# Kernel tuning notes

Measured on AMD Instinct MI355X. Metric: run time of the kernel, lower is better.

## Reference

```python
import jax, jax.numpy as jnp
import numpy as np

B, T, C, HS = 8, 2048, 1024, 64


def setup_inputs() -> dict:
    key = jax.random.key(0)
    ks = jax.random.split(key, 4)
    x = jax.random.normal(ks[0], (B, T, C), dtype=jnp.float32)
    Wq = jax.random.normal(ks[1], (C, HS), dtype=jnp.float32) * (C ** -0.5)
    Wk = jax.random.normal(ks[2], (C, HS), dtype=jnp.float32) * (C ** -0.5)
    Wv = jax.random.normal(ks[3], (C, HS), dtype=jnp.float32) * (C ** -0.5)
    mask = jnp.tril(jnp.ones((T, T), dtype=jnp.int32))  # causal mask
    return {"x": x, "mask": mask, "Wq": Wq, "Wk": Wk, "Wv": Wv}


def reference(x, mask, Wq, Wk, Wv):
    # x: [B,T,C]; bias-free projections to head_size
    q = jnp.einsum("btc,ch->bth", x, Wq)
    k = jnp.einsum("btc,ch->bth", x, Wk)
    v = jnp.einsum("btc,ch->bth", x, Wv)
    # NOTE: original scales by C**-0.5 (n_embd), not head_size**-0.5
    wei = jnp.einsum("bth,bsh->bts", q, k) * (x.shape[-1] ** -0.5)
    wei = jnp.where(mask[None, :, :] == 0, -jnp.inf, wei)
    wei = jax.nn.softmax(wei, axis=-1)
    # dropout is identity in eval / p=0
    out = jnp.einsum("bts,bsh->bth", wei, v)
    return out
```

## Files before the change

kernel.cpp:

```cpp
#include <hip/hip_runtime.h>
#include <hip/hip_bf16.h>


#define B_  8
#define T_  2048
#define C_  1024
#define HS_ 64
#define MROWS (B_ * T_)

typedef __attribute__((ext_vector_type(8))) short bf16x8;
typedef __attribute__((ext_vector_type(4))) float f32x4;
typedef __attribute__((ext_vector_type(4))) float float4v;

#define SCALE_LOG2 0.04508422037445829f

__device__ __forceinline__ short f2bs(float f) {
    __hip_bfloat16 h = __float2bfloat16(f);
    short s;
    __builtin_memcpy(&s, &h, 2);
    return s;
}

__global__ void wt_kernel(const float* __restrict__ Wq,
                          const float* __restrict__ Wk,
                          const float* __restrict__ Wv,
                          __hip_bfloat16* __restrict__ Wt) {
    int m = blockIdx.x >> 6;
    int h = blockIdx.x & 63;
    const float* W = (m == 0) ? Wq : (m == 1) ? Wk : Wv;
    size_t outBase = (size_t)m * (HS_ * C_) + (size_t)h * C_;
    for (int c = threadIdx.x; c < C_; c += blockDim.x)
        Wt[outBase + c] = __float2bfloat16(W[(size_t)c * HS_ + h]);
}

__global__ __launch_bounds__(256) void proj_kernel(
    const float* __restrict__ x,
    const __hip_bfloat16* __restrict__ Wt,
    __hip_bfloat16* __restrict__ Q,
    __hip_bfloat16* __restrict__ Kp,
    __hip_bfloat16* __restrict__ Vt)
{
    const int lane = threadIdx.x & 63;
    const int wave = threadIdx.x >> 6;
    const int quad = lane >> 4;
    const int l15  = lane & 15;
    const int row0 = blockIdx.x * 64;

    f32x4 acc[4][3];
#pragma unroll
    for (int rt = 0; rt < 4; ++rt)
#pragma unroll
        for (int j = 0; j < 3; ++j)
            acc[rt][j] = (f32x4){0.f, 0.f, 0.f, 0.f};

    for (int kc = 0; kc < C_; kc += 32) {
        bf16x8 a[4];
#pragma unroll
        for (int rt = 0; rt < 4; ++rt) {
            const float4v* p = (const float4v*)
                (x + (size_t)(row0 + rt * 16 + l15) * C_ + kc + quad * 8);
            float4v f0 = p[0], f1 = p[1];
#pragma unroll
            for (int j = 0; j < 4; ++j) { a[rt][j] = f2bs(f0[j]); a[rt][4+j] = f2bs(f1[j]); }
        }
        bf16x8 b[3];
#pragma unroll
        for (int j = 0; j < 3; ++j) {
            int nt = wave * 3 + j;
            int h  = ((nt & 3) * 16) + l15;
            b[j] = *(const bf16x8*)(Wt + (size_t)(nt >> 2) * (HS_ * C_) +
                                    (size_t)h * C_ + kc + quad * 8);
        }
#pragma unroll
        for (int rt = 0; rt < 4; ++rt)
#pragma unroll
            for (int j = 0; j < 3; ++j)
                acc[rt][j] = __builtin_amdgcn_mfma_f32_16x16x32_bf16(
                    a[rt], b[j], acc[rt][j], 0, 0, 0);
    }

#pragma unroll
    for (int rt = 0; rt < 4; ++rt) {
#pragma unroll
        for (int j = 0; j < 3; ++j) {
            int nt   = wave * 3 + j;
            int mtx  = nt >> 2;
            int col  = (nt & 3) * 16 + l15;
#pragma unroll
            for (int r = 0; r < 4; ++r) {
                int row = row0 + rt * 16 + quad * 4 + r;
                __hip_bfloat16 v = __float2bfloat16(acc[rt][j][r]);
                if (mtx == 0) {
                    Q[(size_t)row * HS_ + col] = v;
                } else if (mtx == 1) {
                    Kp[(size_t)row * HS_ + col] = v;
                } else {
                    int bidx = row >> 11;
                    int t    = row & 2047;
                    Vt[((size_t)bidx * HS_ + col) * T_ + t] = v;
                }
            }
        }
    }
}

__global__ __launch_bounds__(256) void attn_kernel(
    const __hip_bfloat16* __restrict__ Q,
    const __hip_bfloat16* __restrict__ Kp,
    const __hip_bfloat16* __restrict__ Vt,
    float* __restrict__ out)
{
    __shared__ __align__(16) __hip_bfloat16 plds[4][16 * 32];
    __shared__ float o_lds[4][16][64];
    __shared__ float l_lds[4][16][16];

    const int tid  = threadIdx.x;
    const int wv   = tid >> 6;
    const int lane = tid & 63;
    const int quad = lane >> 4;
    const int l15  = lane & 15;
    const int b    = blockIdx.x & 7;
    const int lt   = 127 - (blockIdx.x >> 3);
    const int qb   = lt * 16;
    const int rowg = b * T_ + qb;

    bf16x8 qf0 = *(const bf16x8*)(Q + (size_t)(rowg + l15) * HS_ + quad * 8);
    bf16x8 qf1 = *(const bf16x8*)(Q + (size_t)(rowg + l15) * HS_ + 32 + quad * 8);

    f32x4 o[4];
#pragma unroll
    for (int j = 0; j < 4; ++j) o[j] = (f32x4){0.f, 0.f, 0.f, 0.f};
    float lp[4] = {0.f, 0.f, 0.f, 0.f};

    __hip_bfloat16* pb = plds[wv];
    const int ntiles = qb / 32 + 1;

    for (int t = wv; t < ntiles; t += 4) {
        const int kb = t * 32;
        const __hip_bfloat16* Kb = Kp + (size_t)(b * T_ + kb) * HS_;
        bf16x8 k0a = *(const bf16x8*)(Kb + (size_t)l15 * HS_ + quad * 8);
        bf16x8 k0b = *(const bf16x8*)(Kb + (size_t)l15 * HS_ + 32 + quad * 8);
        bf16x8 k1a = *(const bf16x8*)(Kb + (size_t)(16 + l15) * HS_ + quad * 8);
        bf16x8 k1b = *(const bf16x8*)(Kb + (size_t)(16 + l15) * HS_ + 32 + quad * 8);

        f32x4 s0 = (f32x4){0.f, 0.f, 0.f, 0.f};
        f32x4 s1 = (f32x4){0.f, 0.f, 0.f, 0.f};
        s0 = __builtin_amdgcn_mfma_f32_16x16x32_bf16(qf0, k0a, s0, 0, 0, 0);
        s0 = __builtin_amdgcn_mfma_f32_16x16x32_bf16(qf1, k0b, s0, 0, 0, 0);
        s1 = __builtin_amdgcn_mfma_f32_16x16x32_bf16(qf0, k1a, s1, 0, 0, 0);
        s1 = __builtin_amdgcn_mfma_f32_16x16x32_bf16(qf1, k1b, s1, 0, 0, 0);

        const bool diag = (kb + 31 > qb);
        float p0[4], p1[4];
#pragma unroll
        for (int r = 0; r < 4; ++r) {
            p0[r] = exp2f(s0[r] * SCALE_LOG2);
            p1[r] = exp2f(s1[r] * SCALE_LOG2);
            if (diag) {
                int row = qb + quad * 4 + r;
                if (kb + l15 > row)      p0[r] = 0.f;
                if (kb + 16 + l15 > row) p1[r] = 0.f;
            }
            lp[r] += p0[r] + p1[r];
        }

#pragma unroll
        for (int r = 0; r < 4; ++r) {
            pb[(quad * 4 + r) * 32 + l15]      = __float2bfloat16(p0[r]);
            pb[(quad * 4 + r) * 32 + 16 + l15] = __float2bfloat16(p1[r]);
        }
        asm volatile("s_waitcnt lgkmcnt(0)" ::: "memory");
        bf16x8 pf = *(const bf16x8*)(pb + l15 * 32 + quad * 8);

#pragma unroll
        for (int j = 0; j < 4; ++j) {
            const __hip_bfloat16* vp =
                Vt + ((size_t)b * HS_ + j * 16 + l15) * T_ + kb + quad * 8;
            bf16x8 vf = *(const bf16x8*)vp;
            o[j] = __builtin_amdgcn_mfma_f32_16x16x32_bf16(pf, vf, o[j], 0, 0, 0);
        }
    }

#pragma unroll
    for (int j = 0; j < 4; ++j)
#pragma unroll
        for (int r = 0; r < 4; ++r)
            o_lds[wv][quad * 4 + r][j * 16 + l15] = o[j][r];
#pragma unroll
    for (int r = 0; r < 4; ++r)
        l_lds[wv][quad * 4 + r][l15] = lp[r];
    __syncthreads();

    if (tid < 16) {
        float s = 0.f;
#pragma unroll
        for (int w = 0; w < 4; ++w)
            for (int c = 0; c < 16; ++c) s += l_lds[w][tid][c];
        l_lds[0][tid][0] = s;
    }
    __syncthreads();

    const int h = tid & 63;
#pragma unroll
    for (int k = 0; k < 4; ++k) {
        int row = (tid >> 6) * 4 + k;
        float s = o_lds[0][row][h] + o_lds[1][row][h] +
                  o_lds[2][row][h] + o_lds[3][row][h];
        out[(size_t)(rowg + row) * HS_ + h] = s / l_lds[0][row][0];
    }
}

extern "C" void kernel_launch(void* const* d_in, const int* in_sizes, int n_in,
                              void* d_out, int out_size, void* d_ws, size_t ws_size,
                              hipStream_t stream) {
    (void)in_sizes; (void)n_in; (void)out_size; (void)ws_size;
    const float* x  = (const float*)d_in[0];
    const float* Wq = (const float*)d_in[2];
    const float* Wk = (const float*)d_in[3];
    const float* Wv = (const float*)d_in[4];

    __hip_bfloat16* ws = (__hip_bfloat16*)d_ws;
    __hip_bfloat16* Wt = ws;
    __hip_bfloat16* Q  = ws + 196608;
    __hip_bfloat16* Kp = ws + 196608 + 1048576;
    __hip_bfloat16* Vt = ws + 196608 + 2 * 1048576;

    wt_kernel<<<192, 256, 0, stream>>>(Wq, Wk, Wv, Wt);
    proj_kernel<<<MROWS / 64, 256, 0, stream>>>(x, Wt, Q, Kp, Vt);
    attn_kernel<<<(T_ / 16) * B_, 256, 0, stream>>>(Q, Kp, Vt, (float*)d_out);
}
```

Baseline: 180.7 us.

## Split projection work across 16 waves, one row tile per wave

The projection kernel now runs 1024 threads per block, and each wave handles a single 16-row tile and three output tiles instead of four row tiles. Each wave's accumulator count drops from 12 to 3, which cuts register pressure and puts more waves in flight to hide load latency. In exchange, each x row tile is loaded and converted by four waves instead of one, and each weight tile is loaded by four waves instead of one. That shifts more traffic onto the cache.

```diff
diff --git a/kernel.cpp b/kernel.cpp
--- a/kernel.cpp
+++ b/kernel.cpp
@@ -33,7 +33,7 @@
         Wt[outBase + c] = __float2bfloat16(W[(size_t)c * HS_ + h]);
 }
 
-__global__ __launch_bounds__(256) void proj_kernel(
+__global__ __launch_bounds__(1024) void proj_kernel(
     const float* __restrict__ x,
     const __hip_bfloat16* __restrict__ Wt,
     __hip_bfloat16* __restrict__ Q,
@@ -42,63 +42,58 @@
 {
     const int lane = threadIdx.x & 63;
     const int wave = threadIdx.x >> 6;
+    const int rt   = wave >> 2;
+    const int ng   = wave & 3;
     const int quad = lane >> 4;
     const int l15  = lane & 15;
     const int row0 = blockIdx.x * 64;
 
-    f32x4 acc[4][3];
-#pragma unroll
-    for (int rt = 0; rt < 4; ++rt)
+    const float* xrow = x + (size_t)(row0 + rt * 16 + l15) * C_ + quad * 8;
+    const __hip_bfloat16* wbase[3];
+#pragma unroll
+    for (int j = 0; j < 3; ++j) {
+        int nt = ng * 3 + j;
+        int h  = ((nt & 3) * 16) + l15;
+        wbase[j] = Wt + (size_t)(nt >> 2) * (HS_ * C_) + (size_t)h * C_ + quad * 8;
+    }
+
+    f32x4 acc[3];
+#pragma unroll
+    for (int j = 0; j < 3; ++j) acc[j] = (f32x4){0.f, 0.f, 0.f, 0.f};
+
+#pragma unroll 2
+    for (int kc = 0; kc < C_; kc += 32) {
+        const float4v* p = (const float4v*)(xrow + kc);
+        float4v f0 = p[0], f1 = p[1];
+        bf16x8 a;
+#pragma unroll
+        for (int j = 0; j < 4; ++j) { a[j] = f2bs(f0[j]); a[4 + j] = f2bs(f1[j]); }
+        bf16x8 b[3];
 #pragma unroll
         for (int j = 0; j < 3; ++j)
-            acc[rt][j] = (f32x4){0.f, 0.f, 0.f, 0.f};
-
-    for (int kc = 0; kc < C_; kc += 32) {
-        bf16x8 a[4];
-#pragma unroll
-        for (int rt = 0; rt < 4; ++rt) {
-            const float4v* p = (const float4v*)
-                (x + (size_t)(row0 + rt * 16 + l15) * C_ + kc + quad * 8);
-            float4v f0 = p[0], f1 = p[1];
-#pragma unroll
-            for (int j = 0; j < 4; ++j) { a[rt][j] = f2bs(f0[j]); a[rt][4+j] = f2bs(f1[j]); }
-        }
-        bf16x8 b[3];
-#pragma unroll
-        for (int j = 0; j < 3; ++j) {
-            int nt = wave * 3 + j;
-            int h  = ((nt & 3) * 16) + l15;
-            b[j] = *(const bf16x8*)(Wt + (size_t)(nt >> 2) * (HS_ * C_) +
-                                    (size_t)h * C_ + kc + quad * 8);
-        }
-#pragma unroll
-        for (int rt = 0; rt < 4; ++rt)
-#pragma unroll
-            for (int j = 0; j < 3; ++j)
-                acc[rt][j] = __builtin_amdgcn_mfma_f32_16x16x32_bf16(
-                    a[rt], b[j], acc[rt][j], 0, 0, 0);
-    }
-
-#pragma unroll
-    for (int rt = 0; rt < 4; ++rt) {
-#pragma unroll
-        for (int j = 0; j < 3; ++j) {
-            int nt   = wave * 3 + j;
-            int mtx  = nt >> 2;
-            int col  = (nt & 3) * 16 + l15;
-#pragma unroll
-            for (int r = 0; r < 4; ++r) {
-                int row = row0 + rt * 16 + quad * 4 + r;
-                __hip_bfloat16 v = __float2bfloat16(acc[rt][j][r]);
-                if (mtx == 0) {
-                    Q[(size_t)row * HS_ + col] = v;
-                } else if (mtx == 1) {
-                    Kp[(size_t)row * HS_ + col] = v;
-                } else {
-                    int bidx = row >> 11;
-                    int t    = row & 2047;
-                    Vt[((size_t)bidx * HS_ + col) * T_ + t] = v;
-                }
+            b[j] = *(const bf16x8*)(wbase[j] + kc);
+#pragma unroll
+        for (int j = 0; j < 3; ++j)
+            acc[j] = __builtin_amdgcn_mfma_f32_16x16x32_bf16(a, b[j], acc[j], 0, 0, 0);
+    }
+
+#pragma unroll
+    for (int j = 0; j < 3; ++j) {
+        int nt   = ng * 3 + j;
+        int mtx  = nt >> 2;
+        int col  = (nt & 3) * 16 + l15;
+#pragma unroll
+        for (int r = 0; r < 4; ++r) {
+            int row = row0 + rt * 16 + quad * 4 + r;
+            __hip_bfloat16 v = __float2bfloat16(acc[j][r]);
+            if (mtx == 0) {
+                Q[(size_t)row * HS_ + col] = v;
+            } else if (mtx == 1) {
+                Kp[(size_t)row * HS_ + col] = v;
+            } else {
+                int bidx = row >> 11;
+                int t    = row & 2047;
+                Vt[((size_t)bidx * HS_ + col) * T_ + t] = v;
             }
         }
     }
@@ -226,6 +221,6 @@
     __hip_bfloat16* Vt = ws + 196608 + 2 * 1048576;
 
     wt_kernel<<<192, 256, 0, stream>>>(Wq, Wk, Wv, Wt);
-    proj_kernel<<<MROWS / 64, 256, 0, stream>>>(x, Wt, Q, Kp, Vt);
+    proj_kernel<<<MROWS / 64, 1024, 0, stream>>>(x, Wt, Q, Kp, Vt);
     attn_kernel<<<(T_ / 16) * B_, 256, 0, stream>>>(Q, Kp, Vt, (float*)d_out);
 }
```

New measurement: 215.6 us. 19.3% more time.

## Stage x through LDS in projection, prefetch K/V in attention, tile weight transpose

Applied to the files above, without the earlier changes.

The projection kernel now stages 32-row x tiles into LDS with global_load_lds, processes 64-wide K chunks, and halves rows per block to double the grid. The attention kernel double-buffers its K and V register fragments so the next tile's loads overlap the current tile's compute. The weight transpose goes through a shared-memory tile so both reads and writes are coalesced. The aim is to cut strided global loads and hide memory latency, at the cost of more registers and extra barriers.

```diff
diff --git a/kernel.cpp b/kernel.cpp
--- a/kernel.cpp
+++ b/kernel.cpp
@@ -21,71 +21,117 @@
     return s;
 }
 
-__global__ void wt_kernel(const float* __restrict__ Wq,
-                          const float* __restrict__ Wk,
-                          const float* __restrict__ Wv,
-                          __hip_bfloat16* __restrict__ Wt) {
-    int m = blockIdx.x >> 6;
-    int h = blockIdx.x & 63;
+__global__ __launch_bounds__(256) void wt_kernel(
+    const float* __restrict__ Wq,
+    const float* __restrict__ Wk,
+    const float* __restrict__ Wv,
+    __hip_bfloat16* __restrict__ Wt) {
+    __shared__ float tile[64][65];
+    const int m  = blockIdx.x >> 4;
+    const int r0 = (blockIdx.x & 15) * 64;
     const float* W = (m == 0) ? Wq : (m == 1) ? Wk : Wv;
-    size_t outBase = (size_t)m * (HS_ * C_) + (size_t)h * C_;
-    for (int c = threadIdx.x; c < C_; c += blockDim.x)
-        Wt[outBase + c] = __float2bfloat16(W[(size_t)c * HS_ + h]);
-}
-
-__global__ __launch_bounds__(256) void proj_kernel(
+    const int i = threadIdx.x >> 6;
+    const int j = threadIdx.x & 63;
+#pragma unroll
+    for (int p = 0; p < 16; ++p) {
+        int r = p * 4 + i;
+        tile[r][j] = W[(size_t)(r0 + r) * HS_ + j];
+    }
+    __syncthreads();
+#pragma unroll
+    for (int p = 0; p < 16; ++p) {
+        int h = p * 4 + i;
+        Wt[(size_t)m * (HS_ * C_) + (size_t)h * C_ + r0 + j] =
+            __float2bfloat16(tile[j][h]);
+    }
+}
+
+__global__ __launch_bounds__(256, 2) void proj_kernel(
     const float* __restrict__ x,
     const __hip_bfloat16* __restrict__ Wt,
     __hip_bfloat16* __restrict__ Q,
     __hip_bfloat16* __restrict__ Kp,
     __hip_bfloat16* __restrict__ Vt)
 {
+    __shared__ float xtile[32 * 68];
+
     const int lane = threadIdx.x & 63;
     const int wave = threadIdx.x >> 6;
     const int quad = lane >> 4;
     const int l15  = lane & 15;
-    const int row0 = blockIdx.x * 64;
-
-    f32x4 acc[4][3];
-#pragma unroll
-    for (int rt = 0; rt < 4; ++rt)
+    const int row0 = blockIdx.x * 32;
+
+    const float* gsrc[8];
+#pragma unroll
+    for (int rr = 0; rr < 8; ++rr)
+        gsrc[rr] = x + (size_t)(row0 + wave * 8 + rr) * C_ + lane;
+
+    const __hip_bfloat16* wbase[3];
+#pragma unroll
+    for (int j = 0; j < 3; ++j) {
+        int nt = wave * 3 + j;
+        int h  = ((nt & 3) * 16) + l15;
+        wbase[j] = Wt + (size_t)(nt >> 2) * (HS_ * C_) + (size_t)h * C_ + quad * 8;
+    }
+
+    f32x4 acc[2][3];
+#pragma unroll
+    for (int rt = 0; rt < 2; ++rt)
 #pragma unroll
         for (int j = 0; j < 3; ++j)
             acc[rt][j] = (f32x4){0.f, 0.f, 0.f, 0.f};
 
-    for (int kc = 0; kc < C_; kc += 32) {
-        bf16x8 a[4];
-#pragma unroll
-        for (int rt = 0; rt < 4; ++rt) {
-            const float4v* p = (const float4v*)
-                (x + (size_t)(row0 + rt * 16 + l15) * C_ + kc + quad * 8);
-            float4v f0 = p[0], f1 = p[1];
-#pragma unroll
-            for (int j = 0; j < 4; ++j) { a[rt][j] = f2bs(f0[j]); a[rt][4+j] = f2bs(f1[j]); }
-        }
-        bf16x8 b[3];
+#pragma unroll 1
+    for (int kc = 0; kc < C_; kc += 64) {
+        if (kc) __syncthreads();
+
+#pragma unroll
+        for (int rr = 0; rr < 8; ++rr)
+            __builtin_amdgcn_global_load_lds(
+                (const __attribute__((address_space(1))) unsigned*)(gsrc[rr] + kc),
+                (__attribute__((address_space(3))) unsigned*)
+                    (&xtile[(wave * 8 + rr) * 68]),
+                4, 0, 0);
+
+        bf16x8 bfr[2][3];
+#pragma unroll
+        for (int ks = 0; ks < 2; ++ks)
+#pragma unroll
+            for (int j = 0; j < 3; ++j)
+                bfr[ks][j] = *(const bf16x8*)(wbase[j] + kc + ks * 32);
+
+        __syncthreads();
+
+#pragma unroll
+        for (int ks = 0; ks < 2; ++ks) {
+            bf16x8 a[2];
+#pragma unroll
+            for (int rt = 0; rt < 2; ++rt) {
+                const float4v* p = (const float4v*)
+                    &xtile[(rt * 16 + l15) * 68 + ks * 32 + quad * 8];
+                float4v f0 = p[0], f1 = p[1];
+#pragma unroll
+                for (int e = 0; e < 4; ++e) {
+                    a[rt][e]     = f2bs(f0[e]);
+                    a[rt][4 + e] = f2bs(f1[e]);
+                }
+            }
+#pragma unroll
+            for (int rt = 0; rt < 2; ++rt)
+#pragma unroll
+                for (int j = 0; j < 3; ++j)
+                    acc[rt][j] = __builtin_amdgcn_mfma_f32_16x16x32_bf16(
+                        a[rt], bfr[ks][j], acc[rt][j], 0, 0, 0);
+        }
+    }
+
+#pragma unroll
+    for (int rt = 0; rt < 2; ++rt) {
 #pragma unroll
         for (int j = 0; j < 3; ++j) {
-            int nt = wave * 3 + j;
-            int h  = ((nt & 3) * 16) + l15;
-            b[j] = *(const bf16x8*)(Wt + (size_t)(nt >> 2) * (HS_ * C_) +
-                                    (size_t)h * C_ + kc + quad * 8);
-        }
-#pragma unroll
-        for (int rt = 0; rt < 4; ++rt)
-#pragma unroll
-            for (int j = 0; j < 3; ++j)
-                acc[rt][j] = __builtin_amdgcn_mfma_f32_16x16x32_bf16(
-                    a[rt], b[j], acc[rt][j], 0, 0, 0);
-    }
-
-#pragma unroll
-    for (int rt = 0; rt < 4; ++rt) {
-#pragma unroll
-        for (int j = 0; j < 3; ++j) {
-            int nt   = wave * 3 + j;
-            int mtx  = nt >> 2;
-            int col  = (nt & 3) * 16 + l15;
+            int nt  = wave * 3 + j;
+            int mtx = nt >> 2;
+            int col = (nt & 3) * 16 + l15;
 #pragma unroll
             for (int r = 0; r < 4; ++r) {
                 int row = row0 + rt * 16 + quad * 4 + r;
@@ -135,20 +181,34 @@
     __hip_bfloat16* pb = plds[wv];
     const int ntiles = qb / 32 + 1;
 
-    for (int t = wv; t < ntiles; t += 4) {
+    auto load_kv = [&](int kb, bf16x8 kf[4], bf16x8 vf[4]) {
+        const __hip_bfloat16* Kb = Kp + (size_t)(b * T_ + kb) * HS_;
+        kf[0] = *(const bf16x8*)(Kb + (size_t)l15 * HS_ + quad * 8);
+        kf[1] = *(const bf16x8*)(Kb + (size_t)l15 * HS_ + 32 + quad * 8);
+        kf[2] = *(const bf16x8*)(Kb + (size_t)(16 + l15) * HS_ + quad * 8);
+        kf[3] = *(const bf16x8*)(Kb + (size_t)(16 + l15) * HS_ + 32 + quad * 8);
+#pragma unroll
+        for (int j = 0; j < 4; ++j)
+            vf[j] = *(const bf16x8*)
+                (Vt + ((size_t)b * HS_ + j * 16 + l15) * T_ + kb + quad * 8);
+    };
+
+    bf16x8 kcur[4], vcur[4], knxt[4], vnxt[4];
+    int t = wv;
+    if (t < ntiles) load_kv(t * 32, kcur, vcur);
+
+#pragma unroll 1
+    for (; t < ntiles; t += 4) {
+        const int tn = t + 4;
+        load_kv(tn < ntiles ? tn * 32 : 0, knxt, vnxt);
+
         const int kb = t * 32;
-        const __hip_bfloat16* Kb = Kp + (size_t)(b * T_ + kb) * HS_;
-        bf16x8 k0a = *(const bf16x8*)(Kb + (size_t)l15 * HS_ + quad * 8);
-        bf16x8 k0b = *(const bf16x8*)(Kb + (size_t)l15 * HS_ + 32 + quad * 8);
-        bf16x8 k1a = *(const bf16x8*)(Kb + (size_t)(16 + l15) * HS_ + quad * 8);
-        bf16x8 k1b = *(const bf16x8*)(Kb + (size_t)(16 + l15) * HS_ + 32 + quad * 8);
-
         f32x4 s0 = (f32x4){0.f, 0.f, 0.f, 0.f};
         f32x4 s1 = (f32x4){0.f, 0.f, 0.f, 0.f};
-        s0 = __builtin_amdgcn_mfma_f32_16x16x32_bf16(qf0, k0a, s0, 0, 0, 0);
-        s0 = __builtin_amdgcn_mfma_f32_16x16x32_bf16(qf1, k0b, s0, 0, 0, 0);
-        s1 = __builtin_amdgcn_mfma_f32_16x16x32_bf16(qf0, k1a, s1, 0, 0, 0);
-        s1 = __builtin_amdgcn_mfma_f32_16x16x32_bf16(qf1, k1b, s1, 0, 0, 0);
+        s0 = __builtin_amdgcn_mfma_f32_16x16x32_bf16(qf0, kcur[0], s0, 0, 0, 0);
+        s0 = __builtin_amdgcn_mfma_f32_16x16x32_bf16(qf1, kcur[1], s0, 0, 0, 0);
+        s1 = __builtin_amdgcn_mfma_f32_16x16x32_bf16(qf0, kcur[2], s1, 0, 0, 0);
+        s1 = __builtin_amdgcn_mfma_f32_16x16x32_bf16(qf1, kcur[3], s1, 0, 0, 0);
 
         const bool diag = (kb + 31 > qb);
         float p0[4], p1[4];
@@ -173,12 +233,11 @@
         bf16x8 pf = *(const bf16x8*)(pb + l15 * 32 + quad * 8);
 
 #pragma unroll
-        for (int j = 0; j < 4; ++j) {
-            const __hip_bfloat16* vp =
-                Vt + ((size_t)b * HS_ + j * 16 + l15) * T_ + kb + quad * 8;
-            bf16x8 vf = *(const bf16x8*)vp;
-            o[j] = __builtin_amdgcn_mfma_f32_16x16x32_bf16(pf, vf, o[j], 0, 0, 0);
-        }
+        for (int j = 0; j < 4; ++j)
+            o[j] = __builtin_amdgcn_mfma_f32_16x16x32_bf16(pf, vcur[j], o[j], 0, 0, 0);
+
+#pragma unroll
+        for (int j = 0; j < 4; ++j) { kcur[j] = knxt[j]; vcur[j] = vnxt[j]; }
     }
 
 #pragma unroll
@@ -225,7 +284,7 @@
     __hip_bfloat16* Kp = ws + 196608 + 1048576;
     __hip_bfloat16* Vt = ws + 196608 + 2 * 1048576;
 
-    wt_kernel<<<192, 256, 0, stream>>>(Wq, Wk, Wv, Wt);
-    proj_kernel<<<MROWS / 64, 256, 0, stream>>>(x, Wt, Q, Kp, Vt);
+    wt_kernel<<<48, 256, 0, stream>>>(Wq, Wk, Wv, Wt);
+    proj_kernel<<<MROWS / 32, 256, 0, stream>>>(x, Wt, Q, Kp, Vt);
     attn_kernel<<<(T_ / 16) * B_, 256, 0, stream>>>(Q, Kp, Vt, (float*)d_out);
 }
```

New measurement: 169.8 us. 6.1% less time.
